# Kernel tuning notes

Hardware: AMD Instinct MI355X
Metric: run time of the kernel (lower is better)

## Reference

```python
import jax, jax.numpy as jnp
import numpy as np

GROUP_SIZE = 128
NIBBLES = 8  # int4 values packed per int32


def dequantize(qweight, qzeros, scales):
    """Unpack int4 weights/zeros and dequantize: w = (q - z) * scale.

    qweight: [in/8, out] int32, 8 int4 values packed along the IN dim.
    qzeros:  [groups, out/8] int32, 8 int4 zeros packed along the OUT dim.
    scales:  [groups, out] fp16.
    Returns w: [in, out] fp16.
    """
    shifts = (jnp.arange(NIBBLES, dtype=jnp.int32) * 4)
    # unpack weights along input dim -> [in/8, 8, out] -> [in, out]
    q = ((qweight[:, None, :] >> shifts[None, :, None]) & 15)
    q = q.reshape(-1, qweight.shape[1])
    # unpack zeros along output dim -> [groups, out/8, 8] -> [groups, out]
    z = ((qzeros[:, :, None] >> shifts[None, None, :]) & 15)
    z = z.reshape(qzeros.shape[0], -1)
    # broadcast per-group zeros/scales to per-input-row
    z_full = jnp.repeat(z, GROUP_SIZE, axis=0).astype(scales.dtype)   # [in, out]
    s_full = jnp.repeat(scales, GROUP_SIZE, axis=0)                    # [in, out]
    return (q.astype(scales.dtype) - z_full) * s_full


def setup_inputs() -> dict:
    key = jax.random.key(0)
    k1, k2, k3, k4, k5 = jax.random.split(key, 5)
    B, S, IN, OUT, G = 2, 2048, 4096, 11008, 32
    x = jax.random.normal(k1, (B, S, IN), dtype=jnp.float16)
    qweight = jax.random.randint(k2, (IN // 8, OUT), 0, 2147483647, dtype=jnp.int32)
    qzeros = jax.random.randint(k3, (G, OUT // 8), 0, 2147483647, dtype=jnp.int32)
    scales = jax.random.uniform(k4, (G, OUT), dtype=jnp.float16, minval=0.001, maxval=0.02)
    bias = jax.random.normal(k5, (OUT,), dtype=jnp.float16)
    return {"x": x, "qweight": qweight, "qzeros": qzeros, "scales": scales, "bias": bias}


def reference(x, qweight, qzeros, scales, bias):
    w = dequantize(qweight, qzeros, scales)  # [in, out] fp16
    # q4_matmul accumulates in fp32, emits fp16
    out = jnp.einsum('bsi,io->bso', x, w, preferred_element_type=jnp.float32)
    out = out.astype(jnp.float16) + bias
    return out
```

## Files before the change

kernel.cpp:

```cpp
#include <hip/hip_runtime.h>
#include <cstdint>
#include <cstddef>


typedef unsigned short u16;
typedef u16    u16x8  __attribute__((ext_vector_type(8)));
typedef __bf16 bfv8   __attribute__((ext_vector_type(8)));
typedef float  f32x4  __attribute__((ext_vector_type(4)));

#define K_DIM 4096
#define N_DIM 11008
#define GS    128
#define KT32N (K_DIM / 32)
#define LSTR  72

__device__ __forceinline__ u16 f2bf(float f) {
  union { float f; uint32_t u; } v;
  v.f = f;
  uint32_t u = v.u + 0x7FFFu + ((v.u >> 16) & 1u);
  return (u16)(u >> 16);
}
__device__ __forceinline__ float f16r(float v) {
  return (float)(_Float16)v;
}
__device__ __forceinline__ void async_load16(const u16* g, u16* l) {
  __builtin_amdgcn_global_load_lds(
      (const __attribute__((address_space(1))) uint32_t*)g,
      (__attribute__((address_space(3))) uint32_t*)l, 16, 0, 0);
}

__global__ __launch_bounds__(256) void convert_x32(
    const float* __restrict__ x, u16* __restrict__ xb) {
  const int kt = blockIdx.x, mt = blockIdx.y;
  const int m0 = mt * 128, k0 = kt * 32;
  u16* dst = xb + ((size_t)mt * KT32N + kt) * 4096;
#pragma unroll
  for (int i = 0; i < 2; ++i) {
    const int g = i * 256 + threadIdx.x;
    const int r = g >> 2, s = g & 3;
    const int kq = s ^ ((r >> 1) & 3);
    const float* sp = x + (size_t)(m0 + r) * K_DIM + (k0 + kq * 8);
    const f32x4 p = *(const f32x4*)sp;
    const f32x4 q = *(const f32x4*)(sp + 4);
    u16x8 o;
#pragma unroll
    for (int t = 0; t < 4; ++t) { o[t] = f2bf(p[t]); o[t + 4] = f2bf(q[t]); }
    *(u16x8*)(dst + (size_t)g * 8) = o;
  }
}

__global__ __launch_bounds__(256) void dequant32(
    const uint32_t* __restrict__ qweight, const uint32_t* __restrict__ qzeros,
    const float* __restrict__ scales, u16* __restrict__ wt) {
  const int kt = blockIdx.x, nt = blockIdx.y;
  const int n0 = nt * 128;
  const int gq = kt >> 2;
  u16* dst = wt + ((size_t)nt * KT32N + kt) * 4096;
#pragma unroll
  for (int i = 0; i < 2; ++i) {
    const int g = i * 256 + threadIdx.x;
    const int r = g >> 2, s = g & 3;
    const int kq = s ^ ((r >> 1) & 3);
    const int n = n0 + r;
    const uint32_t zq = qzeros[(size_t)gq * (N_DIM / 8) + (n >> 3)];
    const int   z   = (int)((zq >> ((n & 7) * 4)) & 15u);
    const float sc  = scales[(size_t)gq * N_DIM + n];
    const float nzs = -sc * (float)z;
    const uint32_t q = qweight[(size_t)(kt * 4 + kq) * N_DIM + n];
    u16x8 o;
#pragma unroll
    for (int t = 0; t < 8; ++t) {
      const int qv = (int)((q >> (t * 4)) & 15u);
      o[t] = f2bf(fmaf((float)qv, sc, nzs));
    }
    *(u16x8*)(dst + (size_t)g * 8) = o;
  }
}

#define LDF(p)  __builtin_bit_cast(bfv8, *(const u16x8*)(p))
#define BAR()   __builtin_amdgcn_s_barrier()
#define VMW_(n) asm volatile("s_waitcnt vmcnt(" #n ")")
#define VMW(n)  VMW_(n)
#define LKW0()  asm volatile("s_waitcnt lgkmcnt(0)")
#define SBAR()  __builtin_amdgcn_sched_barrier(0)

#define STAGE_A32K(ktt, h, dbuf) do {                                         \
    const u16* s_ = at0 + ((size_t)(h) * KT32N + (ktt)) * 4096;               \
    async_load16(s_ + (size_t)tid * 8,                                        \
                 &As[(dbuf) * 8192 + (h) * 4096 + wave * 512]);               \
  } while (0)
#define STAGE_B32K(ktt, h, dbuf) do {                                         \
    const u16* s_ = bt0 + ((size_t)(h) * KT32N + (ktt)) * 4096;               \
    async_load16(s_ + (size_t)tid * 8,                                        \
                 &Bs[(dbuf) * 8192 + (h) * 4096 + wave * 512]);               \
  } while (0)

#define RD_A4(v, ib, bufl) do {                                               \
    _Pragma("unroll")                                                         \
    for (int i_ = 0; i_ < 4; ++i_)                                            \
      v[i_] = LDF(&As[(bufl) * 8192 + aoff + ((ib) + i_) * 512 + kq]);        \
  } while (0)
#define RD_B4(v, bufl) do {                                                   \
    _Pragma("unroll")                                                         \
    for (int j_ = 0; j_ < 4; ++j_)                                            \
      v[j_] = LDF(&Bs[(bufl) * 8192 + boff + j_ * 512 + kq]);                 \
  } while (0)

#define MM16(ib, av, bv) do {                                                 \
    __builtin_amdgcn_s_setprio(1);                                            \
    _Pragma("unroll")                                                         \
    for (int ii_ = 0; ii_ < 4; ++ii_)                                         \
      _Pragma("unroll")                                                       \
      for (int j_ = 0; j_ < 4; ++j_)                                          \
        acc[(ib) + ii_][j_] = __builtin_amdgcn_mfma_f32_16x16x32_bf16(        \
            av[ii_], bv[j_], acc[(ib) + ii_][j_], 0, 0, 0);                   \
    __builtin_amdgcn_s_setprio(0);                                            \
  } while (0)

#define KTILE32(T, BUFL, DO_ST, VMWSTMT) do {                                 \
                                                                 \
    RD_A4(a0, 0, BUFL);                                                       \
    RD_B4(bb, BUFL);                                                          \
    if (DO_ST) {                                                              \
      STAGE_A32K((T) + 2, 0, ((BUFL) + 2) & 3);                               \
      STAGE_A32K((T) + 2, 1, ((BUFL) + 2) & 3);                               \
    }                                                                         \
    SBAR();                                                                   \
    BAR();                                                                    \
    LKW0(); SBAR();                                                           \
    MM16(0, a0, bb);                                                          \
    BAR();                                                                    \
                                                                 \
    RD_A4(a1, 4, BUFL);                                                       \
    if (DO_ST) {                                                              \
      STAGE_B32K((T) + 2, 0, ((BUFL) + 2) & 3);                               \
      STAGE_B32K((T) + 2, 1, ((BUFL) + 2) & 3);                               \
    }                                                                         \
    SBAR();                                                                   \
    BAR();                                                                    \
    LKW0(); SBAR();                                                           \
    MM16(4, a1, bb);                                                          \
    VMWSTMT;                                                                  \
    BAR();                                                                    \
  } while (0)

__global__ __launch_bounds__(512, 2) void gemm_256(
    const u16* __restrict__ xb, const u16* __restrict__ wt,
    const float* __restrict__ bias, float* __restrict__ out) {
  __shared__ __align__(16) u16 As[4 * 8192];
  __shared__ __align__(16) u16 Bs[4 * 8192];

  const int tid  = threadIdx.x;
  const int lane = tid & 63;
  const int wave = tid >> 6;
  const int wm   = wave >> 2;
  const int wn   = wave & 3;
  const int lrow = lane & 15;
  const int lk   = lane >> 4;

  const int nwg = gridDim.x * gridDim.y;
  int wg = blockIdx.y * gridDim.x + blockIdx.x;
  if ((nwg & 7) == 0) wg = (wg & 7) * (nwg >> 3) + (wg >> 3);
  const int bx = wg % gridDim.x;
  const int by = wg / gridDim.x;
  const int n0 = bx * 256;
  const int m0 = by * 256;

  const u16* at0 = xb + (size_t)(2 * by) * KT32N * 4096;
  const u16* bt0 = wt + (size_t)(2 * bx) * KT32N * 4096;

  const int aoff = wm * 4096 + lrow * 32;
  const int boff = (wn >> 1) * 4096 + ((wn & 1) * 64 + lrow) * 32;
  const int kq   = (lk ^ ((lrow >> 1) & 3)) * 8;

  bfv8 a0[4], a1[4], bb[4];
  f32x4 acc[8][4];
#pragma unroll
  for (int i = 0; i < 8; ++i)
#pragma unroll
    for (int j = 0; j < 4; ++j) acc[i][j] = f32x4{0.f, 0.f, 0.f, 0.f};

  STAGE_A32K(0, 0, 0); STAGE_A32K(0, 1, 0);
  STAGE_B32K(0, 0, 0); STAGE_B32K(0, 1, 0);
  STAGE_A32K(1, 0, 1); STAGE_A32K(1, 1, 1);
  STAGE_B32K(1, 0, 1); STAGE_B32K(1, 1, 1);
  VMW(4); BAR();

#pragma unroll 1
  for (int t = 0; t < 124; t += 4) {
    KTILE32(t + 0, 0, 1, VMW(4));
    KTILE32(t + 1, 1, 1, VMW(4));
    KTILE32(t + 2, 2, 1, VMW(4));
    KTILE32(t + 3, 3, 1, VMW(4));
  }
  KTILE32(124, 0, 1, VMW(4));
  KTILE32(125, 1, 1, VMW(4));
  KTILE32(126, 2, 0, VMW(0));
  KTILE32(127, 3, 0, (void)0);

#pragma unroll
  for (int j = 0; j < 4; ++j) {
    const int n = n0 + wn * 64 + j * 16 + lrow;
    const float bvf = bias[n];
#pragma unroll
    for (int i = 0; i < 8; ++i) {
      const int mrow = m0 + wm * 128 + i * 16 + lk * 4;
#pragma unroll
      for (int r = 0; r < 4; ++r) {
        out[(size_t)(mrow + r) * N_DIM + n] = f16r(f16r(acc[i][j][r]) + bvf);
      }
    }
  }
}

__global__ __launch_bounds__(256) void gemm_fused(
    const float* __restrict__ xf, const uint32_t* __restrict__ qw,
    const uint32_t* __restrict__ qzeros, const float* __restrict__ scales,
    const float* __restrict__ bias, float* __restrict__ out) {
  __shared__ __align__(16) u16 As[128 * LSTR];
  __shared__ __align__(16) u16 Bs[128 * LSTR];

  const int tid  = threadIdx.x;
  const int lane = tid & 63;
  const int wave = tid >> 6;
  const int n0 = blockIdx.x * 128;
  const int m0 = blockIdx.y * 128;
  const int m_off = (wave >> 1) * 64;
  const int n_off = (wave & 1) * 64;
  const int lrow  = lane & 15;
  const int lk    = lane >> 4;
  const int sm = tid >> 3;
  const int sc = tid & 7;

  f32x4 acc[4][4];
#pragma unroll
  for (int i = 0; i < 4; ++i)
#pragma unroll
    for (int j = 0; j < 4; ++j) acc[i][j] = f32x4{0.f, 0.f, 0.f, 0.f};

  const int ncol = n0 + (tid & 127);
  float s_cur = 0.f, nzs_cur = 0.f;

  for (int kt = 0; kt < K_DIM / 64; ++kt) {
    const int k0 = kt * 64;
    u16x8 av[4];
#pragma unroll
    for (int i = 0; i < 4; ++i) {
      const int m = i * 32 + sm;
      const float* sp = xf + (size_t)(m0 + m) * K_DIM + (k0 + sc * 8);
      const f32x4 p = *(const f32x4*)sp;
      const f32x4 q4 = *(const f32x4*)(sp + 4);
#pragma unroll
      for (int t = 0; t < 4; ++t) { av[i][t] = f2bf(p[t]); av[i][t+4] = f2bf(q4[t]); }
    }
    u16x8 bv[4];
    if ((k0 & (GS - 1)) == 0) {
      const int g = k0 >> 7;
      const uint32_t zq = qzeros[(size_t)g * (N_DIM / 8) + (ncol >> 3)];
      const int z = (int)((zq >> ((ncol & 7) * 4)) & 15u);
      s_cur = scales[(size_t)g * N_DIM + ncol];
      nzs_cur = -s_cur * (float)z;
    }
#pragma unroll
    for (int i = 0; i < 4; ++i) {
      const int k8l = (tid >> 7) + i * 2;
      const uint32_t q = qw[(size_t)(k0 / 8 + k8l) * N_DIM + ncol];
#pragma unroll
      for (int t = 0; t < 8; ++t) {
        const int qv = (int)((q >> (t * 4)) & 15u);
        bv[i][t] = f2bf(fmaf((float)qv, s_cur, nzs_cur));
      }
    }
#pragma unroll
    for (int i = 0; i < 4; ++i)
      *(u16x8*)&As[(i * 32 + sm) * LSTR + sc * 8] = av[i];
    {
      const int nl = tid & 127;
#pragma unroll
      for (int i = 0; i < 4; ++i) {
        const int k8l = (tid >> 7) + i * 2;
        *(u16x8*)&Bs[nl * LSTR + k8l * 8] = bv[i];
      }
    }
    __syncthreads();
#pragma unroll
    for (int ks = 0; ks < 2; ++ks) {
      const int c = (ks * 4 + lk) * 8;
      bfv8 a[4], b[4];
#pragma unroll
      for (int i = 0; i < 4; ++i)
        a[i] = __builtin_bit_cast(bfv8,
                 *(const u16x8*)&As[(m_off + i * 16 + lrow) * LSTR + c]);
#pragma unroll
      for (int j = 0; j < 4; ++j)
        b[j] = __builtin_bit_cast(bfv8,
                 *(const u16x8*)&Bs[(n_off + j * 16 + lrow) * LSTR + c]);
#pragma unroll
      for (int i = 0; i < 4; ++i)
#pragma unroll
        for (int j = 0; j < 4; ++j)
          acc[i][j] = __builtin_amdgcn_mfma_f32_16x16x32_bf16(a[i], b[j],
                                                              acc[i][j], 0, 0, 0);
    }
    __syncthreads();
  }
#pragma unroll
  for (int j = 0; j < 4; ++j) {
    const int n = n0 + n_off + j * 16 + lrow;
    const float bvf = bias[n];
#pragma unroll
    for (int i = 0; i < 4; ++i) {
      const int mrow = m0 + m_off + i * 16 + lk * 4;
#pragma unroll
      for (int r = 0; r < 4; ++r)
        out[(size_t)(mrow + r) * N_DIM + n] = f16r(f16r(acc[i][j][r]) + bvf);
    }
  }
}

extern "C" void kernel_launch(void* const* d_in, const int* in_sizes, int n_in,
                              void* d_out, int out_size, void* d_ws, size_t ws_size,
                              hipStream_t stream) {
  const float* x = nullptr;      const uint32_t* qweight = nullptr;
  const uint32_t* qzeros = nullptr;
  const float* scales = nullptr; const float* bias = nullptr;
  int M = 4096;
  for (int i = 0; i < n_in; ++i) {
    const long long s = in_sizes[i];
    if      (s == (long long)(K_DIM / 8) * N_DIM) qweight = (const uint32_t*)d_in[i];
    else if (s == (long long)(K_DIM / GS) * (N_DIM / 8)) qzeros = (const uint32_t*)d_in[i];
    else if (s == (long long)(K_DIM / GS) * N_DIM) scales = (const float*)d_in[i];
    else if (s == (long long)N_DIM) bias = (const float*)d_in[i];
    else { x = (const float*)d_in[i]; M = (int)(s / K_DIM); }
  }
  float* out = (float*)d_out;

  const size_t xb_bytes = (size_t)M * K_DIM * sizeof(u16);
  const size_t wt_bytes = (size_t)N_DIM * K_DIM * sizeof(u16);

  if (ws_size >= xb_bytes + wt_bytes && (M % 256) == 0) {
    u16* xbp = (u16*)d_ws;
    u16* wtp = (u16*)((char*)d_ws + xb_bytes);
    convert_x32<<<dim3(KT32N, M / 128), 256, 0, stream>>>(x, xbp);
    dequant32<<<dim3(KT32N, N_DIM / 128), 256, 0, stream>>>(
        qweight, qzeros, scales, wtp);
    gemm_256<<<dim3(N_DIM / 256, M / 256), 512, 0, stream>>>(
        xbp, wtp, bias, out);
  } else {
    gemm_fused<<<dim3(N_DIM / 128, (M + 127) / 128), 256, 0, stream>>>(
        x, qweight, qzeros, scales, bias, out);
  }
}
```

Baseline: 658.2 us.

## Shrink GEMM tile to 128x256 with triple-buffered single-barrier pipeline

Replaces the 256x256 block tile with a 128x256 tile, cutting accumulators from 8x4 to 4x4 per wave. Launch bounds go from 2 to 4 blocks per CU. The shared-memory pipeline goes from four buffers with two barriers per k-step to three buffers with one barrier per step. The intent is higher occupancy and less barrier overhead to hide latency. The cost is lower arithmetic intensity per tile, so A and B are reloaded from global/L2 more often.

```diff
diff --git a/kernel.cpp b/kernel.cpp
--- a/kernel.cpp
+++ b/kernel.cpp
@@ -81,74 +81,42 @@
 #define BAR()   __builtin_amdgcn_s_barrier()
 #define VMW_(n) asm volatile("s_waitcnt vmcnt(" #n ")")
 #define VMW(n)  VMW_(n)
-#define LKW0()  asm volatile("s_waitcnt lgkmcnt(0)")
 #define SBAR()  __builtin_amdgcn_sched_barrier(0)
 
-#define STAGE_A32K(ktt, h, dbuf) do {                                         \
-    const u16* s_ = at0 + ((size_t)(h) * KT32N + (ktt)) * 4096;               \
-    async_load16(s_ + (size_t)tid * 8,                                        \
-                 &As[(dbuf) * 8192 + (h) * 4096 + wave * 512]);               \
+#define STAGE(T, DB) do {                                                     \
+    async_load16(at  + (size_t)(T) * 4096 + tid * 8,                          \
+                 &As[(DB) * 4096 + wave * 512]);                              \
+    async_load16(bt0 + (size_t)(T) * 4096 + tid * 8,                          \
+                 &Bs[(DB) * 8192 + wave * 512]);                              \
+    async_load16(bt1 + (size_t)(T) * 4096 + tid * 8,                          \
+                 &Bs[(DB) * 8192 + 4096 + wave * 512]);                       \
   } while (0)
-#define STAGE_B32K(ktt, h, dbuf) do {                                         \
-    const u16* s_ = bt0 + ((size_t)(h) * KT32N + (ktt)) * 4096;               \
-    async_load16(s_ + (size_t)tid * 8,                                        \
-                 &Bs[(dbuf) * 8192 + (h) * 4096 + wave * 512]);               \
-  } while (0)
-
-#define RD_A4(v, ib, bufl) do {                                               \
+
+#define KT1(T, B0, DO_ST, VMWSTMT) do {                                       \
+    bfv8 a_[4], b_[4];                                                        \
     _Pragma("unroll")                                                         \
     for (int i_ = 0; i_ < 4; ++i_)                                            \
-      v[i_] = LDF(&As[(bufl) * 8192 + aoff + ((ib) + i_) * 512 + kq]);        \
-  } while (0)
-#define RD_B4(v, bufl) do {                                                   \
+      a_[i_] = LDF(&As[(B0) * 4096 + aoff + i_ * 512 + kq]);                  \
     _Pragma("unroll")                                                         \
     for (int j_ = 0; j_ < 4; ++j_)                                            \
-      v[j_] = LDF(&Bs[(bufl) * 8192 + boff + j_ * 512 + kq]);                 \
-  } while (0)
-
-#define MM16(ib, av, bv) do {                                                 \
-    __builtin_amdgcn_s_setprio(1);                                            \
+      b_[j_] = LDF(&Bs[(B0) * 8192 + boff + j_ * 512 + kq]);                  \
+    if (DO_ST) { STAGE((T) + 2, ((B0) + 2) % 3); }                            \
     _Pragma("unroll")                                                         \
-    for (int ii_ = 0; ii_ < 4; ++ii_)                                         \
+    for (int i_ = 0; i_ < 4; ++i_)                                            \
       _Pragma("unroll")                                                       \
       for (int j_ = 0; j_ < 4; ++j_)                                          \
-        acc[(ib) + ii_][j_] = __builtin_amdgcn_mfma_f32_16x16x32_bf16(        \
-            av[ii_], bv[j_], acc[(ib) + ii_][j_], 0, 0, 0);                   \
-    __builtin_amdgcn_s_setprio(0);                                            \
-  } while (0)
-
-#define KTILE32(T, BUFL, DO_ST, VMWSTMT) do {                                 \
-                                                                 \
-    RD_A4(a0, 0, BUFL);                                                       \
-    RD_B4(bb, BUFL);                                                          \
-    if (DO_ST) {                                                              \
-      STAGE_A32K((T) + 2, 0, ((BUFL) + 2) & 3);                               \
-      STAGE_A32K((T) + 2, 1, ((BUFL) + 2) & 3);                               \
-    }                                                                         \
-    SBAR();                                                                   \
-    BAR();                                                                    \
-    LKW0(); SBAR();                                                           \
-    MM16(0, a0, bb);                                                          \
-    BAR();                                                                    \
-                                                                 \
-    RD_A4(a1, 4, BUFL);                                                       \
-    if (DO_ST) {                                                              \
-      STAGE_B32K((T) + 2, 0, ((BUFL) + 2) & 3);                               \
-      STAGE_B32K((T) + 2, 1, ((BUFL) + 2) & 3);                               \
-    }                                                                         \
-    SBAR();                                                                   \
-    BAR();                                                                    \
-    LKW0(); SBAR();                                                           \
-    MM16(4, a1, bb);                                                          \
+        acc[i_][j_] = __builtin_amdgcn_mfma_f32_16x16x32_bf16(                \
+            a_[i_], b_[j_], acc[i_][j_], 0, 0, 0);                            \
     VMWSTMT;                                                                  \
     BAR();                                                                    \
+    SBAR();                                                                   \
   } while (0)
 
-__global__ __launch_bounds__(512, 2) void gemm_256(
+__global__ __launch_bounds__(512, 4) void gemm_128x256(
     const u16* __restrict__ xb, const u16* __restrict__ wt,
     const float* __restrict__ bias, float* __restrict__ out) {
-  __shared__ __align__(16) u16 As[4 * 8192];
-  __shared__ __align__(16) u16 Bs[4 * 8192];
+  __shared__ __align__(16) u16 As[3 * 4096];
+  __shared__ __align__(16) u16 Bs[3 * 8192];
 
   const int tid  = threadIdx.x;
   const int lane = tid & 63;
@@ -164,47 +132,41 @@
   const int bx = wg % gridDim.x;
   const int by = wg / gridDim.x;
   const int n0 = bx * 256;
-  const int m0 = by * 256;
-
-  const u16* at0 = xb + (size_t)(2 * by) * KT32N * 4096;
+  const int m0 = by * 128;
+
+  const u16* at  = xb + (size_t)by * KT32N * 4096;
   const u16* bt0 = wt + (size_t)(2 * bx) * KT32N * 4096;
-
-  const int aoff = wm * 4096 + lrow * 32;
+  const u16* bt1 = wt + (size_t)(2 * bx + 1) * KT32N * 4096;
+
+  const int aoff = wm * 2048 + lrow * 32;
   const int boff = (wn >> 1) * 4096 + ((wn & 1) * 64 + lrow) * 32;
   const int kq   = (lk ^ ((lrow >> 1) & 3)) * 8;
 
-  bfv8 a0[4], a1[4], bb[4];
-  f32x4 acc[8][4];
-#pragma unroll
-  for (int i = 0; i < 8; ++i)
+  f32x4 acc[4][4];
+#pragma unroll
+  for (int i = 0; i < 4; ++i)
 #pragma unroll
     for (int j = 0; j < 4; ++j) acc[i][j] = f32x4{0.f, 0.f, 0.f, 0.f};
 
-  STAGE_A32K(0, 0, 0); STAGE_A32K(0, 1, 0);
-  STAGE_B32K(0, 0, 0); STAGE_B32K(0, 1, 0);
-  STAGE_A32K(1, 0, 1); STAGE_A32K(1, 1, 1);
-  STAGE_B32K(1, 0, 1); STAGE_B32K(1, 1, 1);
-  VMW(4); BAR();
+  STAGE(0, 0); STAGE(1, 1);
+  VMW(3); BAR(); SBAR();
 
 #pragma unroll 1
-  for (int t = 0; t < 124; t += 4) {
-    KTILE32(t + 0, 0, 1, VMW(4));
-    KTILE32(t + 1, 1, 1, VMW(4));
-    KTILE32(t + 2, 2, 1, VMW(4));
-    KTILE32(t + 3, 3, 1, VMW(4));
-  }
-  KTILE32(124, 0, 1, VMW(4));
-  KTILE32(125, 1, 1, VMW(4));
-  KTILE32(126, 2, 0, VMW(0));
-  KTILE32(127, 3, 0, (void)0);
+  for (int t = 0; t < 126; t += 3) {
+    KT1(t + 0, 0, 1, VMW(3));
+    KT1(t + 1, 1, 1, VMW(3));
+    KT1(t + 2, 2, 1, VMW(3));
+  }
+  KT1(126, 0, 0, VMW(0));
+  KT1(127, 1, 0, (void)0);
 
 #pragma unroll
   for (int j = 0; j < 4; ++j) {
     const int n = n0 + wn * 64 + j * 16 + lrow;
     const float bvf = bias[n];
 #pragma unroll
-    for (int i = 0; i < 8; ++i) {
-      const int mrow = m0 + wm * 128 + i * 16 + lk * 4;
+    for (int i = 0; i < 4; ++i) {
+      const int mrow = m0 + wm * 64 + i * 16 + lk * 4;
 #pragma unroll
       for (int r = 0; r < 4; ++r) {
         out[(size_t)(mrow + r) * N_DIM + n] = f16r(f16r(acc[i][j][r]) + bvf);
@@ -338,13 +300,13 @@
   const size_t xb_bytes = (size_t)M * K_DIM * sizeof(u16);
   const size_t wt_bytes = (size_t)N_DIM * K_DIM * sizeof(u16);
 
-  if (ws_size >= xb_bytes + wt_bytes && (M % 256) == 0) {
+  if (ws_size >= xb_bytes + wt_bytes && (M % 128) == 0) {
     u16* xbp = (u16*)d_ws;
     u16* wtp = (u16*)((char*)d_ws + xb_bytes);
     convert_x32<<<dim3(KT32N, M / 128), 256, 0, stream>>>(x, xbp);
     dequant32<<<dim3(KT32N, N_DIM / 128), 256, 0, stream>>>(
         qweight, qzeros, scales, wtp);
-    gemm_256<<<dim3(N_DIM / 256, M / 256), 512, 0, stream>>>(
+    gemm_128x256<<<dim3(N_DIM / 256, M / 128), 512, 0, stream>>>(
         xbp, wtp, bias, out);
   } else {
     gemm_fused<<<dim3(N_DIM / 128, (M + 127) / 128), 256, 0, stream>>>(
```

After: 703.3 us. +6.8%, slower.
